# Kernel optimization log

Measured on AMD Instinct MI355X. Metric: run time of the kernel, lower is better.

Reference implementation:

```python
import jax, jax.numpy as jnp
import numpy as np

EMBED = 768
NHEAD = 12
HEAD_DIM = EMBED // NHEAD


def setup_inputs() -> dict:
    key = jax.random.key(0)
    ks = jax.random.split(key, 6)
    bs, seq = 4, 2048
    x = jax.random.normal(ks[0], (bs, seq, EMBED), dtype=jnp.float32)
    attmask = jax.random.randint(ks[1], (bs, seq), 0, 2, dtype=jnp.int32)
    # xavier-uniform-ish init for weights
    lim_qkv = float(np.sqrt(6.0 / (EMBED + 3 * EMBED)))
    W_qkv = jax.random.uniform(ks[2], (EMBED, 3 * EMBED), minval=-lim_qkv, maxval=lim_qkv, dtype=jnp.float32)
    b_qkv = jnp.zeros((3 * EMBED,), dtype=jnp.float32)
    lim_p = float(np.sqrt(6.0 / (EMBED + EMBED)))
    W_proj = jax.random.uniform(ks[3], (EMBED, EMBED), minval=-lim_p, maxval=lim_p, dtype=jnp.float32)
    b_proj = jnp.zeros((EMBED,), dtype=jnp.float32)
    return {"x": x, "attmask": attmask, "W_qkv": W_qkv, "b_qkv": b_qkv, "W_proj": W_proj, "b_proj": b_proj}


def reference(x, attmask, W_qkv, b_qkv, W_proj, b_proj):
    bs, seq, embed = x.shape
    qkv = x @ W_qkv + b_qkv                     # [bs, seq, 3*embed]
    q, k, v = jnp.split(qkv, 3, axis=-1)
    def to_heads(t):
        return t.reshape(bs, seq, NHEAD, HEAD_DIM).transpose(0, 2, 1, 3)  # [bs, h, seq, d]
    q, k, v = to_heads(q), to_heads(k), to_heads(v)
    scale = 1.0 / np.sqrt(HEAD_DIM).astype(np.float32)
    scores = jnp.einsum('bhqd,bhkd->bhqk', q, k) * scale  # [bs, h, seq, seq]
    mask = (attmask == 0)[:, None, None, :]               # [bs,1,1,seq]
    scores = jnp.where(mask, jnp.asarray(-10000.0, scores.dtype), scores)
    att = jax.nn.softmax(scores, axis=-1)                  # dropout p=0.0 -> identity
    y = jnp.einsum('bhqk,bhkd->bhqd', att, v)              # [bs, h, seq, d]
    y = y.transpose(0, 2, 1, 3).reshape(bs, seq, embed)
    return y @ W_proj + b_proj
```

## Files before the change

### kernel.cpp

```cpp
#include <hip/hip_runtime.h>

typedef unsigned short u16;
typedef unsigned int u32;
typedef __attribute__((ext_vector_type(8))) short short8;
typedef __attribute__((ext_vector_type(4))) short s16x4;
typedef __attribute__((ext_vector_type(4))) float f32x4;

__device__ __forceinline__ float b2f(u16 u) {
    union { u32 i; float f; } v; v.i = ((u32)u) << 16; return v.f;
}
__device__ __forceinline__ u16 f2b(float f) {
    union { u32 i; float f; } v; v.f = f;
    u32 u = v.i;
    return (u16)((u + 0x7FFFu + ((u >> 16) & 1u)) >> 16);
}
__device__ __forceinline__ f32x4 zero4() {
    f32x4 v; v[0] = 0.f; v[1] = 0.f; v[2] = 0.f; v[3] = 0.f; return v;
}
__device__ __forceinline__ u32 cvtpk(float lo, float hi) {
    u32 d;
    asm("v_cvt_pk_bf16_f32 %0, %1, %2" : "=v"(d) : "v"(lo), "v"(hi));
    return d;
}
__device__ __forceinline__ float fexp2(float x) {
#if __has_builtin(__builtin_amdgcn_exp2f)
    return __builtin_amdgcn_exp2f(x);
#else
    return __expf(x * 0.6931471805599453f);
#endif
}
__device__ __forceinline__ void gload16(const u16* g, u16* l) {
    __builtin_amdgcn_global_load_lds(
        (const __attribute__((address_space(1))) u32*)g,
        (__attribute__((address_space(3))) u32*)l, 16, 0, 0);
}

__global__ void convert_kernel(const float* __restrict__ src, u16* __restrict__ dst,
                               int n8) {
    const int stride = gridDim.x * blockDim.x;
    for (int i = blockIdx.x * blockDim.x + threadIdx.x; i < n8; i += stride) {
        const float* s = src + (size_t)i * 8;
        float4 a = ((const float4*)s)[0];
        float4 b = ((const float4*)s)[1];
        short8 o;
        o[0] = (short)f2b(a.x); o[1] = (short)f2b(a.y);
        o[2] = (short)f2b(a.z); o[3] = (short)f2b(a.w);
        o[4] = (short)f2b(b.x); o[5] = (short)f2b(b.y);
        o[6] = (short)f2b(b.z); o[7] = (short)f2b(b.w);
        ((short8*)dst)[i] = o;
    }
}

__global__ void tconvert_kernel(const float* __restrict__ src, u16* __restrict__ dst,
                                int K, int N) {
    __shared__ u16 T[64][72];
    const int n0 = blockIdx.x * 64, k0 = blockIdx.y * 64;
    const int tid = threadIdx.x;
    const int r = tid >> 3, cq = tid & 7;
#pragma unroll
    for (int half = 0; half < 2; half++) {
        const int k = k0 + half * 32 + r;
        const float* s = &src[(size_t)k * N + n0 + cq * 8];
        const float4 f0 = ((const float4*)s)[0];
        const float4 f1 = ((const float4*)s)[1];
        T[cq * 8 + 0][half * 32 + r] = f2b(f0.x);
        T[cq * 8 + 1][half * 32 + r] = f2b(f0.y);
        T[cq * 8 + 2][half * 32 + r] = f2b(f0.z);
        T[cq * 8 + 3][half * 32 + r] = f2b(f0.w);
        T[cq * 8 + 4][half * 32 + r] = f2b(f1.x);
        T[cq * 8 + 5][half * 32 + r] = f2b(f1.y);
        T[cq * 8 + 6][half * 32 + r] = f2b(f1.z);
        T[cq * 8 + 7][half * 32 + r] = f2b(f1.w);
    }
    __syncthreads();
#pragma unroll
    for (int half = 0; half < 2; half++) {
        const int n = half * 32 + r;
        short8 o = *(const short8*)&T[n][cq * 8];
        *(short8*)&dst[(size_t)(n0 + n) * K + k0 + cq * 8] = o;
    }
}

template <int MODE>
__global__ __launch_bounds__(256, 2) void gemm_bt_kernel(
    const u16* __restrict__ A, const u16* __restrict__ Bt,
    const float* __restrict__ bias,
    u16* __restrict__ O0, u16* __restrict__ O1, u16* __restrict__ O2,
    float* __restrict__ Of,
    int M, int N, int K)
{
    __shared__ u16 As[128 * 32];
    __shared__ u16 Bs[128 * 32];

    const int tid = threadIdx.x;
    const int nwgx = gridDim.x;
    const int nwg = nwgx * gridDim.y;
    int lin = blockIdx.y * nwgx + blockIdx.x;
    lin = (lin & 7) * (nwg >> 3) + (lin >> 3);
    const int m0 = (lin / nwgx) * 128, n0 = (lin % nwgx) * 128;
    const int lane = tid & 63, w = tid >> 6;
    const int quad = lane >> 4, c = lane & 15;
    const int wm = (w & 1) * 64, wn = (w >> 1) * 64;

    f32x4 acc[4][4];
#pragma unroll
    for (int i = 0; i < 4; i++)
#pragma unroll
        for (int j = 0; j < 4; j++) acc[i][j] = zero4();

    const int grow = w * 32 + (lane >> 2);
    const int gcol = (lane & 3) * 8;
    const size_t abase = (size_t)(m0 + grow) * K + gcol;
    const size_t bbase = (size_t)(n0 + grow) * K + gcol;
    u16* asl = &As[w * 1024];
    u16* bsl = &Bs[w * 1024];

    for (int k0 = 0; k0 < K; k0 += 32) {
        __syncthreads();
        gload16(A + abase + k0, asl);
        gload16(A + abase + (size_t)16 * K + k0, asl + 512);
        gload16(Bt + bbase + k0, bsl);
        gload16(Bt + bbase + (size_t)16 * K + k0, bsl + 512);
        asm volatile("s_waitcnt vmcnt(0)" ::: "memory");
        __syncthreads();

        short8 af[4], bfr[4];
#pragma unroll
        for (int mi = 0; mi < 4; mi++)
            af[mi] = *(const short8*)&As[(wm + mi * 16 + c) * 32 + quad * 8];
#pragma unroll
        for (int ni = 0; ni < 4; ni++)
            bfr[ni] = *(const short8*)&Bs[(wn + ni * 16 + c) * 32 + quad * 8];
#pragma unroll
        for (int mi = 0; mi < 4; mi++)
#pragma unroll
            for (int ni = 0; ni < 4; ni++)
                acc[mi][ni] = __builtin_amdgcn_mfma_f32_16x16x32_bf16(
                    af[mi], bfr[ni], acc[mi][ni], 0, 0, 0);
    }

#pragma unroll
    for (int ni = 0; ni < 4; ni++) {
        const int gc = n0 + wn + ni * 16 + c;
        const float bv = bias[gc];
        if (MODE == 0) {
            const int which = gc / 768;
            const int e = gc - which * 768;
            const int hh = e >> 6, d = e & 63;
            u16* op = (which == 0) ? O0 : (which == 1 ? O1 : O2);
#pragma unroll
            for (int mi = 0; mi < 4; mi++)
#pragma unroll
                for (int r = 0; r < 4; r++) {
                    const int gr = m0 + wm + mi * 16 + quad * 4 + r;
                    const int bb = gr >> 11, s = gr & 2047;
                    op[(((size_t)bb * 12 + hh) * 2048 + s) * 64 + d] =
                        f2b(acc[mi][ni][r] + bv);
                }
        } else {
#pragma unroll
            for (int mi = 0; mi < 4; mi++)
#pragma unroll
                for (int r = 0; r < 4; r++) {
                    const int gr = m0 + wm + mi * 16 + quad * 4 + r;
                    Of[(size_t)gr * N + gc] = acc[mi][ni][r] + bv;
                }
        }
    }
}

__global__ __launch_bounds__(256) void attn_kernel(
    const u16* __restrict__ Q, const u16* __restrict__ Kv,
    const u16* __restrict__ Vv, const int* __restrict__ attmask,
    u16* __restrict__ Y)
{
    const int S = 2048, D = 64, NH = 12;
    __shared__ u16 Ks[64][72];
    __shared__ u16 Vs[64][68];
    __shared__ u16 Ps[4][16][72];
    __shared__ float msf[2048];

    const int tid = threadIdx.x;
    const int w = tid >> 6, lane = tid & 63;
    const int quad = lane >> 4, c = lane & 15;
    const int bh = blockIdx.x;
    const int qt = blockIdx.y;
    const int b = bh / NH, h = bh - b * NH;

    const u16* Qh = Q + (size_t)bh * S * D;
    const u16* Kh = Kv + (size_t)bh * S * D;
    const u16* Vh = Vv + (size_t)bh * S * D;
    const int q0 = qt * 64 + w * 16;

    short8 aq0 = *(const short8*)&Qh[(size_t)(q0 + c) * D + quad * 8];
    short8 aq1 = *(const short8*)&Qh[(size_t)(q0 + c) * D + 32 + quad * 8];

    for (int i = tid; i < S; i += 256)
        msf[i] = (attmask[b * S + i] == 0) ? -43282.0f : 0.0f;

    f32x4 o_acc[4];
#pragma unroll
    for (int i = 0; i < 4; i++) o_acc[i] = zero4();
    float l = 0.f;

    const int kpos = tid >> 2, kd = (tid & 3) * 8;
    const int p2 = tid >> 3, vd = (tid & 7) * 8;

    short8 k0r = *(const short8*)&Kh[(size_t)kpos * D + kd];
    short8 k1r = *(const short8*)&Kh[(size_t)kpos * D + kd + 32];
    short8 v0r = *(const short8*)&Vh[(size_t)(2 * p2) * D + vd];
    short8 v1r = *(const short8*)&Vh[(size_t)(2 * p2 + 1) * D + vd];

    const float SC = 0.18033688f;

    for (int kt = 0; kt < S / 64; kt++) {
        asm volatile("" ::: "memory");
        __builtin_amdgcn_s_barrier();
        asm volatile("" ::: "memory");
        *(short8*)&Ks[kpos][kd] = k0r;
        *(short8*)&Ks[kpos][kd + 32] = k1r;
#pragma unroll
        for (int j = 0; j < 8; j++) {
            u32 pk = (u32)(u16)v0r[j] | ((u32)(u16)v1r[j] << 16);
            *(u32*)&Vs[vd + j][2 * p2] = pk;
        }
        if (kt + 1 < S / 64) {
            const int nb = (kt + 1) * 64;
            k0r = *(const short8*)&Kh[(size_t)(nb + kpos) * D + kd];
            k1r = *(const short8*)&Kh[(size_t)(nb + kpos) * D + kd + 32];
            v0r = *(const short8*)&Vh[(size_t)(nb + 2 * p2) * D + vd];
            v1r = *(const short8*)&Vh[(size_t)(nb + 2 * p2 + 1) * D + vd];
        }
        asm volatile("s_waitcnt lgkmcnt(0)" ::: "memory");
        __builtin_amdgcn_s_barrier();
        asm volatile("" ::: "memory");

        const int kbase = kt * 64;

        f32x4 s_acc[4];
#pragma unroll
        for (int ni = 0; ni < 4; ni++) s_acc[ni] = zero4();
        __builtin_amdgcn_s_setprio(1);
#pragma unroll
        for (int ni = 0; ni < 4; ni++) {
            short8 bk0 = *(const short8*)&Ks[ni * 16 + c][quad * 8];
            short8 bk1 = *(const short8*)&Ks[ni * 16 + c][32 + quad * 8];
            s_acc[ni] = __builtin_amdgcn_mfma_f32_16x16x32_bf16(bk0, aq0, s_acc[ni], 0, 0, 0);
            s_acc[ni] = __builtin_amdgcn_mfma_f32_16x16x32_bf16(bk1, aq1, s_acc[ni], 0, 0, 0);
        }
        __builtin_amdgcn_s_setprio(0);

#pragma unroll
        for (int ni = 0; ni < 4; ni++) {
            const f32x4 bias = *(const f32x4*)&msf[kbase + ni * 16 + quad * 4];
            float p0 = fexp2(fmaf(s_acc[ni][0], SC, bias[0]));
            float p1 = fexp2(fmaf(s_acc[ni][1], SC, bias[1]));
            float p2f = fexp2(fmaf(s_acc[ni][2], SC, bias[2]));
            float p3 = fexp2(fmaf(s_acc[ni][3], SC, bias[3]));
            l += (p0 + p1) + (p2f + p3);
            uint2 pk;
            pk.x = cvtpk(p0, p1);
            pk.y = cvtpk(p2f, p3);
            *(uint2*)&Ps[w][c][ni * 16 + quad * 4] = pk;
        }

        short8 ap0 = *(const short8*)&Ps[w][c][quad * 8];
        short8 ap1 = *(const short8*)&Ps[w][c][32 + quad * 8];
        __builtin_amdgcn_s_setprio(1);
#pragma unroll
        for (int ni = 0; ni < 4; ni++) {
            union { short8 v8; s16x4 v4[2]; } u0, u1;
            u0.v4[0] = *(const s16x4*)&Vs[ni * 16 + c][quad * 8];
            u0.v4[1] = *(const s16x4*)&Vs[ni * 16 + c][quad * 8 + 4];
            u1.v4[0] = *(const s16x4*)&Vs[ni * 16 + c][32 + quad * 8];
            u1.v4[1] = *(const s16x4*)&Vs[ni * 16 + c][32 + quad * 8 + 4];
            o_acc[ni] = __builtin_amdgcn_mfma_f32_16x16x32_bf16(ap0, u0.v8, o_acc[ni], 0, 0, 0);
            o_acc[ni] = __builtin_amdgcn_mfma_f32_16x16x32_bf16(ap1, u1.v8, o_acc[ni], 0, 0, 0);
        }
        __builtin_amdgcn_s_setprio(0);
    }

    l += __shfl_xor(l, 16);
    l += __shfl_xor(l, 32);

    const size_t ybase = ((size_t)b * S) * 768 + h * 64;
#pragma unroll
    for (int r = 0; r < 4; r++) {
        const float lr = __shfl(l, quad * 4 + r);
        const float inv = 1.f / fmaxf(lr, 1e-30f);
        const int srow = qt * 64 + w * 16 + quad * 4 + r;
#pragma unroll
        for (int ni = 0; ni < 4; ni++)
            Y[ybase + (size_t)srow * 768 + ni * 16 + c] = f2b(o_acc[ni][r] * inv);
    }
}

extern "C" void kernel_launch(void* const* d_in, const int* in_sizes, int n_in,
                              void* d_out, int out_size, void* d_ws, size_t ws_size,
                              hipStream_t stream) {
    const float* x     = (const float*)d_in[0];
    const int* attmask = (const int*)d_in[1];
    const float* Wqkv  = (const float*)d_in[2];
    const float* bqkv  = (const float*)d_in[3];
    const float* Wproj = (const float*)d_in[4];
    const float* bproj = (const float*)d_in[5];
    float* outf = (float*)d_out;

    u16* base = (u16*)d_ws;
    const size_t nx = 4ull * 2048 * 768;
    const size_t nwqkv = 768ull * 2304;
    const size_t nwproj = 768ull * 768;
    u16* xb     = base;
    u16* Wqkvb  = xb + nx;
    u16* Wprojb = Wqkvb + nwqkv;
    u16* Qb     = Wprojb + nwproj;
    const size_t headElems = 48ull * 2048 * 64;
    u16* Kb = Qb + headElems;
    u16* Vb = Kb + headElems;
    u16* Yb = Vb + headElems;

    {
        int n8 = (int)(nx / 8);
        int blocks = (n8 + 255) / 256;
        if (blocks > 1024) blocks = 1024;
        convert_kernel<<<blocks, 256, 0, stream>>>(x, xb, n8);
    }
    tconvert_kernel<<<dim3(2304 / 64, 768 / 64), 256, 0, stream>>>(Wqkv, Wqkvb, 768, 2304);
    tconvert_kernel<<<dim3(768 / 64, 768 / 64), 256, 0, stream>>>(Wproj, Wprojb, 768, 768);

    gemm_bt_kernel<0><<<dim3(18, 64), 256, 0, stream>>>(
        xb, Wqkvb, bqkv, Qb, Kb, Vb, nullptr, 8192, 2304, 768);
    attn_kernel<<<dim3(48, 32), 256, 0, stream>>>(Qb, Kb, Vb, attmask, Yb);
    gemm_bt_kernel<1><<<dim3(6, 64), 256, 0, stream>>>(
        Yb, Wprojb, bproj, nullptr, nullptr, nullptr, outf, 8192, 768, 768);
}
```

Measured before the change: 268.4 us.

## Process two query tiles per attention block to reuse K/V staging

Each attention workgroup now handles 128 query rows instead of 64. Every wave keeps two 16-row Q fragments and reuses each K/V tile loaded into shared memory for both of them, which halves global K/V traffic and staging barriers per query. The grid is halved to 768 blocks, and a launch-bounds occupancy hint of 3 is added. The cost is doubled accumulator registers and fewer blocks, which may reduce occupancy and tail balance.

```diff
diff --git a/kernel.cpp b/kernel.cpp
--- a/kernel.cpp
+++ b/kernel.cpp
@@ -169,7 +169,7 @@
     }
 }
 
-__global__ __launch_bounds__(256) void attn_kernel(
+__global__ __launch_bounds__(256, 3) void attn_kernel(
     const u16* __restrict__ Q, const u16* __restrict__ Kv,
     const u16* __restrict__ Vv, const int* __restrict__ attmask,
     u16* __restrict__ Y)
@@ -177,7 +177,7 @@
     const int S = 2048, D = 64, NH = 12;
     __shared__ u16 Ks[64][72];
     __shared__ u16 Vs[64][68];
-    __shared__ u16 Ps[4][16][72];
+    __shared__ u16 Ps[4][2][16][72];
     __shared__ float msf[2048];
 
     const int tid = threadIdx.x;
@@ -190,18 +190,22 @@
     const u16* Qh = Q + (size_t)bh * S * D;
     const u16* Kh = Kv + (size_t)bh * S * D;
     const u16* Vh = Vv + (size_t)bh * S * D;
-    const int q0 = qt * 64 + w * 16;
-
-    short8 aq0 = *(const short8*)&Qh[(size_t)(q0 + c) * D + quad * 8];
-    short8 aq1 = *(const short8*)&Qh[(size_t)(q0 + c) * D + 32 + quad * 8];
+    const int q0 = qt * 128 + w * 16;
+
+    short8 aq00 = *(const short8*)&Qh[(size_t)(q0 + c) * D + quad * 8];
+    short8 aq01 = *(const short8*)&Qh[(size_t)(q0 + c) * D + 32 + quad * 8];
+    short8 aq10 = *(const short8*)&Qh[(size_t)(q0 + 64 + c) * D + quad * 8];
+    short8 aq11 = *(const short8*)&Qh[(size_t)(q0 + 64 + c) * D + 32 + quad * 8];
 
     for (int i = tid; i < S; i += 256)
         msf[i] = (attmask[b * S + i] == 0) ? -43282.0f : 0.0f;
 
-    f32x4 o_acc[4];
-#pragma unroll
-    for (int i = 0; i < 4; i++) o_acc[i] = zero4();
-    float l = 0.f;
+    f32x4 o_acc[2][4];
+#pragma unroll
+    for (int g = 0; g < 2; g++)
+#pragma unroll
+        for (int i = 0; i < 4; i++) o_acc[g][i] = zero4();
+    float l0 = 0.f, l1 = 0.f;
 
     const int kpos = tid >> 2, kd = (tid & 3) * 8;
     const int p2 = tid >> 3, vd = (tid & 7) * 8;
@@ -237,35 +241,52 @@
 
         const int kbase = kt * 64;
 
-        f32x4 s_acc[4];
-#pragma unroll
-        for (int ni = 0; ni < 4; ni++) s_acc[ni] = zero4();
+        f32x4 s0[4], s1[4];
+#pragma unroll
+        for (int ni = 0; ni < 4; ni++) { s0[ni] = zero4(); s1[ni] = zero4(); }
         __builtin_amdgcn_s_setprio(1);
 #pragma unroll
         for (int ni = 0; ni < 4; ni++) {
             short8 bk0 = *(const short8*)&Ks[ni * 16 + c][quad * 8];
             short8 bk1 = *(const short8*)&Ks[ni * 16 + c][32 + quad * 8];
-            s_acc[ni] = __builtin_amdgcn_mfma_f32_16x16x32_bf16(bk0, aq0, s_acc[ni], 0, 0, 0);
-            s_acc[ni] = __builtin_amdgcn_mfma_f32_16x16x32_bf16(bk1, aq1, s_acc[ni], 0, 0, 0);
+            s0[ni] = __builtin_amdgcn_mfma_f32_16x16x32_bf16(bk0, aq00, s0[ni], 0, 0, 0);
+            s0[ni] = __builtin_amdgcn_mfma_f32_16x16x32_bf16(bk1, aq01, s0[ni], 0, 0, 0);
+            s1[ni] = __builtin_amdgcn_mfma_f32_16x16x32_bf16(bk0, aq10, s1[ni], 0, 0, 0);
+            s1[ni] = __builtin_amdgcn_mfma_f32_16x16x32_bf16(bk1, aq11, s1[ni], 0, 0, 0);
         }
         __builtin_amdgcn_s_setprio(0);
 
 #pragma unroll
         for (int ni = 0; ni < 4; ni++) {
             const f32x4 bias = *(const f32x4*)&msf[kbase + ni * 16 + quad * 4];
-            float p0 = fexp2(fmaf(s_acc[ni][0], SC, bias[0]));
-            float p1 = fexp2(fmaf(s_acc[ni][1], SC, bias[1]));
-            float p2f = fexp2(fmaf(s_acc[ni][2], SC, bias[2]));
-            float p3 = fexp2(fmaf(s_acc[ni][3], SC, bias[3]));
-            l += (p0 + p1) + (p2f + p3);
-            uint2 pk;
-            pk.x = cvtpk(p0, p1);
-            pk.y = cvtpk(p2f, p3);
-            *(uint2*)&Ps[w][c][ni * 16 + quad * 4] = pk;
-        }
-
-        short8 ap0 = *(const short8*)&Ps[w][c][quad * 8];
-        short8 ap1 = *(const short8*)&Ps[w][c][32 + quad * 8];
+            {
+                float p0 = fexp2(fmaf(s0[ni][0], SC, bias[0]));
+                float p1 = fexp2(fmaf(s0[ni][1], SC, bias[1]));
+                float p2f = fexp2(fmaf(s0[ni][2], SC, bias[2]));
+                float p3 = fexp2(fmaf(s0[ni][3], SC, bias[3]));
+                l0 += (p0 + p1) + (p2f + p3);
+                uint2 pk;
+                pk.x = cvtpk(p0, p1);
+                pk.y = cvtpk(p2f, p3);
+                *(uint2*)&Ps[w][0][c][ni * 16 + quad * 4] = pk;
+            }
+            {
+                float p0 = fexp2(fmaf(s1[ni][0], SC, bias[0]));
+                float p1 = fexp2(fmaf(s1[ni][1], SC, bias[1]));
+                float p2f = fexp2(fmaf(s1[ni][2], SC, bias[2]));
+                float p3 = fexp2(fmaf(s1[ni][3], SC, bias[3]));
+                l1 += (p0 + p1) + (p2f + p3);
+                uint2 pk;
+                pk.x = cvtpk(p0, p1);
+                pk.y = cvtpk(p2f, p3);
+                *(uint2*)&Ps[w][1][c][ni * 16 + quad * 4] = pk;
+            }
+        }
+
+        short8 ap00 = *(const short8*)&Ps[w][0][c][quad * 8];
+        short8 ap01 = *(const short8*)&Ps[w][0][c][32 + quad * 8];
+        short8 ap10 = *(const short8*)&Ps[w][1][c][quad * 8];
+        short8 ap11 = *(const short8*)&Ps[w][1][c][32 + quad * 8];
         __builtin_amdgcn_s_setprio(1);
 #pragma unroll
         for (int ni = 0; ni < 4; ni++) {
@@ -274,24 +295,33 @@
             u0.v4[1] = *(const s16x4*)&Vs[ni * 16 + c][quad * 8 + 4];
             u1.v4[0] = *(const s16x4*)&Vs[ni * 16 + c][32 + quad * 8];
             u1.v4[1] = *(const s16x4*)&Vs[ni * 16 + c][32 + quad * 8 + 4];
-            o_acc[ni] = __builtin_amdgcn_mfma_f32_16x16x32_bf16(ap0, u0.v8, o_acc[ni], 0, 0, 0);
-            o_acc[ni] = __builtin_amdgcn_mfma_f32_16x16x32_bf16(ap1, u1.v8, o_acc[ni], 0, 0, 0);
+            o_acc[0][ni] = __builtin_amdgcn_mfma_f32_16x16x32_bf16(ap00, u0.v8, o_acc[0][ni], 0, 0, 0);
+            o_acc[0][ni] = __builtin_amdgcn_mfma_f32_16x16x32_bf16(ap01, u1.v8, o_acc[0][ni], 0, 0, 0);
+            o_acc[1][ni] = __builtin_amdgcn_mfma_f32_16x16x32_bf16(ap10, u0.v8, o_acc[1][ni], 0, 0, 0);
+            o_acc[1][ni] = __builtin_amdgcn_mfma_f32_16x16x32_bf16(ap11, u1.v8, o_acc[1][ni], 0, 0, 0);
         }
         __builtin_amdgcn_s_setprio(0);
     }
 
-    l += __shfl_xor(l, 16);
-    l += __shfl_xor(l, 32);
+    l0 += __shfl_xor(l0, 16);
+    l0 += __shfl_xor(l0, 32);
+    l1 += __shfl_xor(l1, 16);
+    l1 += __shfl_xor(l1, 32);
 
     const size_t ybase = ((size_t)b * S) * 768 + h * 64;
 #pragma unroll
     for (int r = 0; r < 4; r++) {
-        const float lr = __shfl(l, quad * 4 + r);
-        const float inv = 1.f / fmaxf(lr, 1e-30f);
-        const int srow = qt * 64 + w * 16 + quad * 4 + r;
-#pragma unroll
-        for (int ni = 0; ni < 4; ni++)
-            Y[ybase + (size_t)srow * 768 + ni * 16 + c] = f2b(o_acc[ni][r] * inv);
+        const float lr0 = __shfl(l0, quad * 4 + r);
+        const float lr1 = __shfl(l1, quad * 4 + r);
+        const float inv0 = 1.f / fmaxf(lr0, 1e-30f);
+        const float inv1 = 1.f / fmaxf(lr1, 1e-30f);
+        const int srow0 = qt * 128 + w * 16 + quad * 4 + r;
+        const int srow1 = srow0 + 64;
+#pragma unroll
+        for (int ni = 0; ni < 4; ni++) {
+            Y[ybase + (size_t)srow0 * 768 + ni * 16 + c] = f2b(o_acc[0][ni][r] * inv0);
+            Y[ybase + (size_t)srow1 * 768 + ni * 16 + c] = f2b(o_acc[1][ni][r] * inv1);
+        }
     }
 }
 
@@ -330,7 +360,7 @@
 
     gemm_bt_kernel<0><<<dim3(18, 64), 256, 0, stream>>>(
         xb, Wqkvb, bqkv, Qb, Kb, Vb, nullptr, 8192, 2304, 768);
-    attn_kernel<<<dim3(48, 32), 256, 0, stream>>>(Qb, Kb, Vb, attmask, Yb);
+    attn_kernel<<<dim3(48, 16), 256, 0, stream>>>(Qb, Kb, Vb, attmask, Yb);
     gemm_bt_kernel<1><<<dim3(6, 64), 256, 0, stream>>>(
         Yb, Wprojb, bproj, nullptr, nullptr, nullptr, outf, 8192, 768, 768);
 }
```

New measurement: 238.4 us. 11.2% less time.
